# Performance work log

Hardware: AMD Instinct MI355X
Metric: run time of the kernel (lower is better)

## Reference

```python
import jax, jax.numpy as jnp
from jax import lax
import numpy as np

# Fixed 3x3 kernels (PyTorch Conv2d = cross-correlation; lax conv is also cross-correlation, no flip)
GAUSS = jnp.array([[0.0625, 0.125, 0.0625], [0.125, 0.25, 0.125], [0.0625, 0.125, 0.0625]], jnp.float32)
SOBEL_X = jnp.array([[-1., -2., -1.], [0., 0., 0.], [1., 2., 1.]], jnp.float32)
SOBEL_Y = jnp.array([[-1., 0., 1.], [-2., 0., 2.], [-1., 0., 1.]], jnp.float32)
PREWITT_X = jnp.array([[1., 1., 1.], [0., 0., 0.], [-1., -1., -1.]], jnp.float32)
PREWITT_Y = jnp.array([[-1., 0., 1.], [-1., 0., 1.], [-1., 0., 1.]], jnp.float32)
ROBERTS_X = jnp.array([[-1., 0., 0.], [0., 1., 0.], [0., 0., 0.]], jnp.float32)
ROBERTS_Y = jnp.array([[0., -1., 0.], [1., 0., 0.], [0., 0., 0.]], jnp.float32)
LAPLACE = jnp.array([[2., 0., 2.], [0., -8., 0.], [2., 0., 2.]], jnp.float32)


def conv3x3_reflect(x, k):
    # x: [B,1,H,W]; reflect pad by 1 then VALID conv (matches padding='same', padding_mode='reflect')
    xp = jnp.pad(x, ((0, 0), (0, 0), (1, 1), (1, 1)), mode='reflect')
    return lax.conv_general_dilated(xp, k[None, None], (1, 1), 'VALID',
                                    dimension_numbers=('NCHW', 'OIHW', 'NCHW'))


def edge_response(x, k):
    # clip(|conv(x)|, 0, 255).round()  (jnp.round = round-half-even, same as torch)
    return jnp.round(jnp.clip(jnp.abs(conv3x3_reflect(x, k)), 0.0, 255.0))


def add_weighted(a, b):
    # AddWeighted(a, 0.5, b, 0.5, 0.0)
    return jnp.round(0.5 * a + 0.5 * b)


def setup_inputs() -> dict:
    key = jax.random.key(0)
    pan = jax.random.uniform(key, (2, 1, 2048, 2048), dtype=jnp.float32)
    return {"pan": pan}


def reference(pan):
    pan_lp = conv3x3_reflect(pan, GAUSS)
    norm = jnp.max(pan_lp, axis=(1, 2, 3), keepdims=True)  # [B,1,1,1]
    pan_lp = pan_lp * 255.0 / norm
    scale = norm / 255.0

    sobel = add_weighted(edge_response(pan_lp, SOBEL_X), edge_response(pan_lp, SOBEL_Y)) * scale

    pan_lp_f = jnp.floor(pan_lp)  # pan_lp // 1.0
    prewitt = add_weighted(edge_response(pan_lp_f, PREWITT_X), edge_response(pan_lp_f, PREWITT_Y)) * scale
    roberts = add_weighted(edge_response(pan_lp_f, ROBERTS_X), edge_response(pan_lp_f, ROBERTS_Y)) * scale
    laplacian = edge_response(pan_lp_f, LAPLACE) * scale

    # forward differences with replicate (edge) padding on left / top
    pan_pad_x = jnp.pad(pan, ((0, 0), (0, 0), (0, 0), (1, 0)), mode='edge')
    pan_pad_y = jnp.pad(pan, ((0, 0), (0, 0), (1, 0), (0, 0)), mode='edge')
    diff_x = pan_pad_x[:, :, :, 1:] - pan_pad_x[:, :, :, :-1]
    diff_y = pan_pad_y[:, :, 1:, :] - pan_pad_y[:, :, :-1, :]

    return jnp.concatenate([diff_y, diff_x, roberts, prewitt, sobel, laplacian], axis=1)
```

## Files before the change

### kernel.cpp

```cpp
#include <hip/hip_runtime.h>

#define HH 2048
#define WW 2048
#define NB 2
#define FEPS 5e-4f

#define BX 64
#define BY 8
#define SPH (BY + 4)
#define SPW (BX + 4)
#define SPP (SPW + 1)
#define SSH (BY + 2)
#define SSW (BX + 2)
#define SSP (SSW + 1)

__device__ __forceinline__ int refl(int i, int n) {
    if (i < 0) return -i;
    if (i >= n) return 2 * n - 2 - i;
    return i;
}

__device__ __forceinline__ float fastrcp(float x) {
#if __has_builtin(__builtin_amdgcn_rcpf)
    return __builtin_amdgcn_rcpf(x);
#else
    return 1.0f / x;
#endif
}

__device__ __forceinline__ float gauss9_f64(float p00, float p01, float p02,
                                            float p10, float p11, float p12,
                                            float p20, float p21, float p22) {
    const double a = 0.0625 * ((double)p00 + (double)p02 + (double)p20 + (double)p22)
                   + 0.125  * ((double)p01 + (double)p10 + (double)p12 + (double)p21)
                   + 0.25   * (double)p11;
    return (float)a;
}

__global__ void init_norm_kernel(unsigned int* nb) {
    if (threadIdx.x < NB) nb[threadIdx.x] = 0u;
}

__global__ __launch_bounds__(256) void gauss_max_kernel(const float* __restrict__ pan,
                                                        unsigned int* __restrict__ norm_bits) {
    const int b = blockIdx.y;
    const float* __restrict__ img = pan + (size_t)b * HH * WW;
    float lmax = 0.0f;
    const int npix = HH * WW;
    for (int p = blockIdx.x * blockDim.x + threadIdx.x; p < npix; p += gridDim.x * blockDim.x) {
        const int i = p >> 11;
        const int j = p & (WW - 1);
        const int im = refl(i - 1, HH), ip = refl(i + 1, HH);
        const int jm = refl(j - 1, WW), jp = refl(j + 1, WW);
        const float g = gauss9_f64(img[im * WW + jm], img[im * WW + j], img[im * WW + jp],
                                   img[i  * WW + jm], img[i  * WW + j], img[i  * WW + jp],
                                   img[ip * WW + jm], img[ip * WW + j], img[ip * WW + jp]);
        lmax = fmaxf(lmax, g);
    }
    #pragma unroll
    for (int off = 32; off > 0; off >>= 1)
        lmax = fmaxf(lmax, __shfl_down(lmax, off, 64));
    __shared__ float smax[4];
    const int lane = threadIdx.x & 63, wid = threadIdx.x >> 6;
    if (lane == 0) smax[wid] = lmax;
    __syncthreads();
    if (threadIdx.x == 0) {
        const float m = fmaxf(fmaxf(smax[0], smax[1]), fmaxf(smax[2], smax[3]));
        atomicMax(norm_bits + b, __float_as_uint(m));
    }
}

__device__ __forceinline__ void epilogue(const float s[3][3], float scale,
                                         float pc, float pup, float pleft,
                                         int i, int j, int b, float* __restrict__ out) {
    float f[3][3];
    #pragma unroll
    for (int di = 0; di < 3; ++di)
        #pragma unroll
        for (int dj = 0; dj < 3; ++dj)
            f[di][dj] = floorf(s[di][dj]);

    const float sx = (s[2][0] + 2.0f * s[2][1] + s[2][2])
                   - (s[0][0] + 2.0f * s[0][1] + s[0][2]);
    const float sy = (s[0][2] + 2.0f * s[1][2] + s[2][2])
                   - (s[0][0] + 2.0f * s[1][0] + s[2][0]);
    const float ex = rintf(fminf(fabsf(sx), 255.0f));
    const float ey = rintf(fminf(fabsf(sy), 255.0f));
    const float sob = rintf(0.5f * ex + 0.5f * ey);

    const float px = (f[0][0] + f[0][1] + f[0][2]) - (f[2][0] + f[2][1] + f[2][2]);
    const float py = (f[0][2] + f[1][2] + f[2][2]) - (f[0][0] + f[1][0] + f[2][0]);
    const float epx = rintf(fminf(fabsf(px), 255.0f));
    const float epy = rintf(fminf(fabsf(py), 255.0f));
    const float prew = rintf(0.5f * epx + 0.5f * epy);

    const float rx = f[1][1] - f[0][0];
    const float ry = f[1][0] - f[0][1];
    const float erx = rintf(fminf(fabsf(rx), 255.0f));
    const float ery = rintf(fminf(fabsf(ry), 255.0f));
    const float rob = rintf(0.5f * erx + 0.5f * ery);

    float el;
    {
        const float fr11 = s[1][1] - f[1][1];
        const int um = (fr11 < FEPS) || (fr11 > 1.0f - FEPS);
        const float m0 = (um && fr11 < FEPS) ? f[1][1] - 1.0f : f[1][1];

        float S0 = 0.0f; int nu = 0;
        {
            const float fr = s[0][0] - f[0][0];
            const int u = (fr < FEPS) || (fr > 1.0f - FEPS);
            S0 += (u && fr < FEPS) ? f[0][0] - 1.0f : f[0][0]; nu += u;
        }
        {
            const float fr = s[0][2] - f[0][2];
            const int u = (fr < FEPS) || (fr > 1.0f - FEPS);
            S0 += (u && fr < FEPS) ? f[0][2] - 1.0f : f[0][2]; nu += u;
        }
        {
            const float fr = s[2][0] - f[2][0];
            const int u = (fr < FEPS) || (fr > 1.0f - FEPS);
            S0 += (u && fr < FEPS) ? f[2][0] - 1.0f : f[2][0]; nu += u;
        }
        {
            const float fr = s[2][2] - f[2][2];
            const int u = (fr < FEPS) || (fr > 1.0f - FEPS);
            S0 += (u && fr < FEPS) ? f[2][2] - 1.0f : f[2][2]; nu += u;
        }

        if ((um | nu) == 0) {
            const float tt = 2.0f * S0 - 8.0f * m0;
            el = rintf(fminf(fabsf(tt), 255.0f));
        } else {
            float Lmin = 1e30f, Lmax = -1e30f;
            for (int mm = 0; mm <= um; ++mm) {
                const float mval = m0 + (float)mm;
                for (int jj = 0; jj <= nu; ++jj) {
                    const float tt = 2.0f * (S0 + (float)jj) - 8.0f * mval;
                    const float L = rintf(fminf(fabsf(tt), 255.0f));
                    Lmin = fminf(Lmin, L);
                    Lmax = fmaxf(Lmax, L);
                }
            }
            el = 0.5f * (Lmin + Lmax);
        }
    }

    const float dy = (i > 0) ? __fsub_rn(pc, pup) : 0.0f;
    const float dx = (j > 0) ? __fsub_rn(pc, pleft) : 0.0f;

    const size_t plane = (size_t)HH * WW;
    const size_t base = ((size_t)(b * 6) * HH + i) * WW + j;
    out[base]             = dy;
    out[base + plane]     = dx;
    out[base + 2 * plane] = __fmul_rn(rob,  scale);
    out[base + 3 * plane] = __fmul_rn(prew, scale);
    out[base + 4 * plane] = __fmul_rn(sob,  scale);
    out[base + 5 * plane] = __fmul_rn(el,   scale);
}

__global__ __launch_bounds__(512) void fused_kernel(const float* __restrict__ pan,
                                                    const unsigned int* __restrict__ norm_bits,
                                                    float* __restrict__ out) {
    __shared__ float sp[SPH][SPP];
    __shared__ float ss[SSH][SSP];

    const int b  = blockIdx.z;
    const int bi = blockIdx.y * BY;
    const int bj = blockIdx.x * BX;
    const float* __restrict__ img = pan + (size_t)b * HH * WW;
    const int tx = threadIdx.x, ty = threadIdx.y;
    const int tid = ty * BX + tx;

    const float norm = __uint_as_float(norm_bits[b]);

    const bool interior = (blockIdx.x >= 1) & (blockIdx.x <= (WW / BX) - 2) &
                          (blockIdx.y >= 1) & (blockIdx.y <= (HH / BY) - 2);
    if (interior) {
        const int r = tid >> 5;
        const int q = tid & 31;
        if (r < SPH && q < 18) {
            const float* rowp = img + (size_t)(bi - 2 + r) * WW + (bj - 4 + 4 * q);
            const float4 v = *(const float4*)rowp;
            const int c0 = 4 * q - 2;
            if (q == 0) {
                sp[r][0] = v.z; sp[r][1] = v.w;
            } else if (q == 17) {
                sp[r][66] = v.x; sp[r][67] = v.y;
            } else {
                sp[r][c0] = v.x; sp[r][c0 + 1] = v.y;
                sp[r][c0 + 2] = v.z; sp[r][c0 + 3] = v.w;
            }
        }
    } else {
        for (int idx = tid; idx < SPH * SPW; idx += BX * BY) {
            const int rr = idx / SPW, cc = idx % SPW;
            sp[rr][cc] = img[refl(bi - 2 + rr, HH) * WW + refl(bj - 2 + cc, WW)];
        }
    }
    __syncthreads();

    const float rnorm = fastrcp(norm);
    for (int idx = tid; idx < SSH * SSW; idx += BX * BY) {
        const int r = idx / SSW, c = idx % SSW;
        const float g = gauss9_f64(sp[r][c],   sp[r][c+1],   sp[r][c+2],
                                   sp[r+1][c], sp[r+1][c+1], sp[r+1][c+2],
                                   sp[r+2][c], sp[r+2][c+1], sp[r+2][c+2]);
        ss[r][c] = __fmul_rn(__fmul_rn(g, 255.0f), rnorm);
    }
    __syncthreads();

    const float scale = __fmul_rn(norm, (1.0f / 255.0f));
    const int i = bi + ty, j = bj + tx;

    float s[3][3];
    #pragma unroll
    for (int di = 0; di < 3; ++di)
        #pragma unroll
        for (int dj = 0; dj < 3; ++dj)
            s[di][dj] = ss[ty + di][tx + dj];

    const float pc    = sp[ty + 2][tx + 2];
    const float pup   = sp[ty + 1][tx + 2];
    const float pleft = sp[ty + 2][tx + 1];

    epilogue(s, scale, pc, pup, pleft, i, j, b, out);
}

extern "C" void kernel_launch(void* const* d_in, const int* in_sizes, int n_in,
                              void* d_out, int out_size, void* d_ws, size_t ws_size,
                              hipStream_t stream) {
    const float* pan = (const float*)d_in[0];
    float* out = (float*)d_out;
    unsigned int* norm_bits = (unsigned int*)d_ws;

    hipLaunchKernelGGL(init_norm_kernel, dim3(1), dim3(64), 0, stream, norm_bits);
    hipLaunchKernelGGL(gauss_max_kernel, dim3(1024, NB), dim3(256), 0, stream, pan, norm_bits);
    dim3 grid(WW / BX, HH / BY, NB);
    dim3 block(BX, BY);
    hipLaunchKernelGGL(fused_kernel, grid, block, 0, stream, pan, norm_bits, out);
}
```

Before: 86.28 us.

## Fuse max reduction and edge filters into one cooperative kernel with grid sync

```diff
diff --git a/kernel.cpp b/kernel.cpp
--- a/kernel.cpp
+++ b/kernel.cpp
@@ -1,18 +1,21 @@
 #include <hip/hip_runtime.h>
+#include <hip/hip_cooperative_groups.h>
+
+namespace cg = cooperative_groups;
 
 #define HH 2048
 #define WW 2048
 #define NB 2
 #define FEPS 5e-4f
 
-#define BX 64
-#define BY 8
-#define SPH (BY + 4)
-#define SPW (BX + 4)
-#define SPP (SPW + 1)
-#define SSH (BY + 2)
-#define SSW (BX + 2)
-#define SSP (SSW + 1)
+#define WS 128
+#define HS 64
+#define GH (HS + 2)
+#define GW (WS + 2)
+#define GP (GW + 1)
+#define SXN (WW / WS)
+#define SYN (HH / HS)
+#define NBLK (SXN * SYN * NB)
 
 __device__ __forceinline__ int refl(int i, int n) {
     if (i < 0) return -i;
@@ -39,35 +42,6 @@
 
 __global__ void init_norm_kernel(unsigned int* nb) {
     if (threadIdx.x < NB) nb[threadIdx.x] = 0u;
-}
-
-__global__ __launch_bounds__(256) void gauss_max_kernel(const float* __restrict__ pan,
-                                                        unsigned int* __restrict__ norm_bits) {
-    const int b = blockIdx.y;
-    const float* __restrict__ img = pan + (size_t)b * HH * WW;
-    float lmax = 0.0f;
-    const int npix = HH * WW;
-    for (int p = blockIdx.x * blockDim.x + threadIdx.x; p < npix; p += gridDim.x * blockDim.x) {
-        const int i = p >> 11;
-        const int j = p & (WW - 1);
-        const int im = refl(i - 1, HH), ip = refl(i + 1, HH);
-        const int jm = refl(j - 1, WW), jp = refl(j + 1, WW);
-        const float g = gauss9_f64(img[im * WW + jm], img[im * WW + j], img[im * WW + jp],
-                                   img[i  * WW + jm], img[i  * WW + j], img[i  * WW + jp],
-                                   img[ip * WW + jm], img[ip * WW + j], img[ip * WW + jp]);
-        lmax = fmaxf(lmax, g);
-    }
-    #pragma unroll
-    for (int off = 32; off > 0; off >>= 1)
-        lmax = fmaxf(lmax, __shfl_down(lmax, off, 64));
-    __shared__ float smax[4];
-    const int lane = threadIdx.x & 63, wid = threadIdx.x >> 6;
-    if (lane == 0) smax[wid] = lmax;
-    __syncthreads();
-    if (threadIdx.x == 0) {
-        const float m = fmaxf(fmaxf(smax[0], smax[1]), fmaxf(smax[2], smax[3]));
-        atomicMax(norm_bits + b, __float_as_uint(m));
-    }
 }
 
 __device__ __forceinline__ void epilogue(const float s[3][3], float scale,
@@ -159,72 +133,78 @@
     out[base + 5 * plane] = __fmul_rn(el,   scale);
 }
 
-__global__ __launch_bounds__(512) void fused_kernel(const float* __restrict__ pan,
-                                                    const unsigned int* __restrict__ norm_bits,
-                                                    float* __restrict__ out) {
-    __shared__ float sp[SPH][SPP];
-    __shared__ float ss[SSH][SSP];
-
-    const int b  = blockIdx.z;
-    const int bi = blockIdx.y * BY;
-    const int bj = blockIdx.x * BX;
+__global__ __launch_bounds__(256, 4) void mega_kernel(const float* __restrict__ pan,
+                                                      unsigned int* __restrict__ norm_bits,
+                                                      float* __restrict__ out) {
+    __shared__ float gl[GH][GP];
+    __shared__ float smax[4];
+
+    const int sid = blockIdx.x;
+    const int b   = sid >> 9;
+    const int t   = sid & 511;
+    const int bj  = (t & (SXN - 1)) * WS;
+    const int bi  = (t >> 4) * HS;
     const float* __restrict__ img = pan + (size_t)b * HH * WW;
-    const int tx = threadIdx.x, ty = threadIdx.y;
-    const int tid = ty * BX + tx;
-
-    const float norm = __uint_as_float(norm_bits[b]);
-
-    const bool interior = (blockIdx.x >= 1) & (blockIdx.x <= (WW / BX) - 2) &
-                          (blockIdx.y >= 1) & (blockIdx.y <= (HH / BY) - 2);
-    if (interior) {
-        const int r = tid >> 5;
-        const int q = tid & 31;
-        if (r < SPH && q < 18) {
-            const float* rowp = img + (size_t)(bi - 2 + r) * WW + (bj - 4 + 4 * q);
-            const float4 v = *(const float4*)rowp;
-            const int c0 = 4 * q - 2;
-            if (q == 0) {
-                sp[r][0] = v.z; sp[r][1] = v.w;
-            } else if (q == 17) {
-                sp[r][66] = v.x; sp[r][67] = v.y;
-            } else {
-                sp[r][c0] = v.x; sp[r][c0 + 1] = v.y;
-                sp[r][c0 + 2] = v.z; sp[r][c0 + 3] = v.w;
-            }
-        }
-    } else {
-        for (int idx = tid; idx < SPH * SPW; idx += BX * BY) {
-            const int rr = idx / SPW, cc = idx % SPW;
-            sp[rr][cc] = img[refl(bi - 2 + rr, HH) * WW + refl(bj - 2 + cc, WW)];
-        }
-    }
+    const int tid = threadIdx.x;
+
+    float lmax = 0.0f;
+    for (int idx = tid; idx < GH * GW; idx += 256) {
+        const int r = idx / GW, c = idx % GW;
+        const int gi = bi - 1 + r, gj = bj - 1 + c;
+        const int i0 = refl(gi - 1, HH), i1 = refl(gi, HH), i2 = refl(gi + 1, HH);
+        const int j0 = refl(gj - 1, WW), j1 = refl(gj, WW), j2 = refl(gj + 1, WW);
+        const float g = gauss9_f64(img[i0 * WW + j0], img[i0 * WW + j1], img[i0 * WW + j2],
+                                   img[i1 * WW + j0], img[i1 * WW + j1], img[i1 * WW + j2],
+                                   img[i2 * WW + j0], img[i2 * WW + j1], img[i2 * WW + j2]);
+        gl[r][c] = g;
+        if (r >= 1 && r < GH - 1 && c >= 1 && c < GW - 1)
+            lmax = fmaxf(lmax, g);
+    }
+
+    #pragma unroll
+    for (int off = 32; off > 0; off >>= 1)
+        lmax = fmaxf(lmax, __shfl_down(lmax, off, 64));
+    const int lane = tid & 63, wid = tid >> 6;
+    if (lane == 0) smax[wid] = lmax;
     __syncthreads();
-
+    if (tid == 0) {
+        const float m = fmaxf(fmaxf(smax[0], smax[1]), fmaxf(smax[2], smax[3]));
+        atomicMax(norm_bits + b, __float_as_uint(m));
+    }
+
+    __threadfence();
+    cg::this_grid().sync();
+
+    const float norm = __uint_as_float(
+        __hip_atomic_load(norm_bits + b, __ATOMIC_RELAXED, __HIP_MEMORY_SCOPE_AGENT));
     const float rnorm = fastrcp(norm);
-    for (int idx = tid; idx < SSH * SSW; idx += BX * BY) {
-        const int r = idx / SSW, c = idx % SSW;
-        const float g = gauss9_f64(sp[r][c],   sp[r][c+1],   sp[r][c+2],
-                                   sp[r+1][c], sp[r+1][c+1], sp[r+1][c+2],
-                                   sp[r+2][c], sp[r+2][c+1], sp[r+2][c+2]);
-        ss[r][c] = __fmul_rn(__fmul_rn(g, 255.0f), rnorm);
+    const float scale = __fmul_rn(norm, (1.0f / 255.0f));
+
+    for (int idx = tid; idx < GH * GW; idx += 256) {
+        const int r = idx / GW, c = idx % GW;
+        gl[r][c] = __fmul_rn(__fmul_rn(gl[r][c], 255.0f), rnorm);
     }
     __syncthreads();
 
-    const float scale = __fmul_rn(norm, (1.0f / 255.0f));
-    const int i = bi + ty, j = bj + tx;
-
-    float s[3][3];
-    #pragma unroll
-    for (int di = 0; di < 3; ++di)
+    for (int p = tid; p < HS * WS; p += 256) {
+        const int r = p >> 7, c = p & (WS - 1);
+        const int i = bi + r, j = bj + c;
+
+        float s[3][3];
         #pragma unroll
-        for (int dj = 0; dj < 3; ++dj)
-            s[di][dj] = ss[ty + di][tx + dj];
-
-    const float pc    = sp[ty + 2][tx + 2];
-    const float pup   = sp[ty + 1][tx + 2];
-    const float pleft = sp[ty + 2][tx + 1];
-
-    epilogue(s, scale, pc, pup, pleft, i, j, b, out);
+        for (int di = 0; di < 3; ++di)
+            #pragma unroll
+            for (int dj = 0; dj < 3; ++dj)
+                s[di][dj] = gl[r + di][c + dj];
+
+        const float pc    = img[(size_t)i * WW + j];
+        const int   iu    = (i > 0) ? i - 1 : 0;
+        const int   jl    = (j > 0) ? j - 1 : 0;
+        const float pup   = img[(size_t)iu * WW + j];
+        const float pleft = img[(size_t)i * WW + jl];
+
+        epilogue(s, scale, pc, pup, pleft, i, j, b, out);
+    }
 }
 
 extern "C" void kernel_launch(void* const* d_in, const int* in_sizes, int n_in,
@@ -235,8 +215,7 @@
     unsigned int* norm_bits = (unsigned int*)d_ws;
 
     hipLaunchKernelGGL(init_norm_kernel, dim3(1), dim3(64), 0, stream, norm_bits);
-    hipLaunchKernelGGL(gauss_max_kernel, dim3(1024, NB), dim3(256), 0, stream, pan, norm_bits);
-    dim3 grid(WW / BX, HH / BY, NB);
-    dim3 block(BX, BY);
-    hipLaunchKernelGGL(fused_kernel, grid, block, 0, stream, pan, norm_bits, out);
-}
+
+    void* args[] = { (void*)&pan, (void*)&norm_bits, (void*)&out };
+    hipLaunchCooperativeKernel((void*)mega_kernel, dim3(NBLK), dim3(256), args, 0, stream);
+}
```

Result: slower. 245.9 us (+185.1%).
